# Kernel tuning notes

Hardware: AMD Instinct MI355X
Metric: run time of the kernel (lower is better)

The kernel has to match this reference:

```python
import jax, jax.numpy as jnp
import numpy as np

N_SEG = 16384      # number of ragged segments (customers)
SEG_LEN = 1024     # events per segment (uniform here; math supports ragged)
N = N_SEG * SEG_LEN
EPS = 1e-5


def setup_inputs() -> dict:
    key = jax.random.key(0)
    k1, k2 = jax.random.split(key)
    # tau = detached model prediction of next inter-event time; must be > 0
    tau = jax.random.uniform(k1, (N,), jnp.float32, 0.1, 2.0)
    # dt = observed inter-event times (non-negative)
    dt = jax.random.uniform(k2, (N,), jnp.float32, 0.0, 1.0)
    # offsets: B+1 boundaries of the ragged segments within the flat arrays
    offsets = jnp.arange(N_SEG + 1, dtype=jnp.int32) * SEG_LEN
    return {"tau": tau, "dt": dt, "offsets": offsets}


def reference(tau, dt, offsets):
    # Original loop: per segment, drop first and last event, accumulate
    # -log_prob under Exponential(rate=1/tau):
    #   -log_prob(x) = log(tau) + (dt + eps) / tau
    # Replaced by a single masked elementwise pass + sum: interior mask is
    # everything except each segment's first index and last index.
    n = dt.shape[0]
    mask = (
        jnp.ones((n,), dtype=bool)
        .at[offsets[:-1]].set(False)      # segment starts
        .at[offsets[1:] - 1].set(False)   # segment ends
    )
    tau_sg = jax.lax.stop_gradient(tau)   # y_pred['next_dt'].detach()
    nll = jnp.log(tau_sg) + (dt + EPS) / tau_sg
    loss = jnp.sum(jnp.where(mask, nll, jnp.zeros((), nll.dtype)))
    final_loss = loss / offsets.shape[0]  # divide by B+1, as in source
    return final_loss
```

## Files before the change

### kernel.cpp

```cpp
#include <hip/hip_runtime.h>

typedef float f32x4 __attribute__((ext_vector_type(4)));

#define EPS 1e-5f
#define THREADS 256
#define MAIN_BLOCKS 2048
#define SUPER 2048
#define BND_THREADS 256

#define GLOAD(dst, addr) \
  asm volatile("global_load_dwordx4 %0, %1, off" : "=v"(dst) : "v"(addr) : "memory")

#define SWAIT(n) \
  asm volatile("s_waitcnt vmcnt(" #n ")" ::: "memory"); \
  __builtin_amdgcn_sched_barrier(0)

#define NLL4(T, E) \
  a0 += __logf(T.x) + __fdividef(E.x + EPS, T.x); \
  a1 += __logf(T.y) + __fdividef(E.y + EPS, T.y); \
  a2 += __logf(T.z) + __fdividef(E.z + EPS, T.z); \
  a3 += __logf(T.w) + __fdividef(E.w + EPS, T.w)

#define ISSUE(T, E, P, Q) \
  GLOAD(T##0, P + 0 * THREADS); GLOAD(E##0, Q + 0 * THREADS); \
  GLOAD(T##1, P + 1 * THREADS); GLOAD(E##1, Q + 1 * THREADS); \
  GLOAD(T##2, P + 2 * THREADS); GLOAD(E##2, Q + 2 * THREADS); \
  GLOAD(T##3, P + 3 * THREADS); GLOAD(E##3, Q + 3 * THREADS); \
  GLOAD(T##4, P + 4 * THREADS); GLOAD(E##4, Q + 4 * THREADS); \
  GLOAD(T##5, P + 5 * THREADS); GLOAD(E##5, Q + 5 * THREADS); \
  GLOAD(T##6, P + 6 * THREADS); GLOAD(E##6, Q + 6 * THREADS); \
  GLOAD(T##7, P + 7 * THREADS); GLOAD(E##7, Q + 7 * THREADS)

#define COMPUTE16(T, E) \
  SWAIT(28); NLL4(T##0, E##0); NLL4(T##1, E##1); \
  SWAIT(24); NLL4(T##2, E##2); NLL4(T##3, E##3); \
  SWAIT(20); NLL4(T##4, E##4); NLL4(T##5, E##5); \
  SWAIT(16); NLL4(T##6, E##6); NLL4(T##7, E##7)

#define COMPUTE0(T, E) \
  SWAIT(12); NLL4(T##0, E##0); NLL4(T##1, E##1); \
  SWAIT(8);  NLL4(T##2, E##2); NLL4(T##3, E##3); \
  SWAIT(4);  NLL4(T##4, E##4); NLL4(T##5, E##5); \
  SWAIT(0);  NLL4(T##6, E##6); NLL4(T##7, E##7)

__global__ __launch_bounds__(THREADS, 2) void tau_loss_main(
    const f32x4* __restrict__ t4,
    const f32x4* __restrict__ d4,
    const float* __restrict__ tau,
    const float* __restrict__ dt,
    float* __restrict__ ws,
    int n) {
    const int n4 = n >> 2;
    const int nsuper = n4 / SUPER;

    float a0 = 0.f, a1 = 0.f, a2 = 0.f, a3 = 0.f;

    f32x4 tA0, tA1, tA2, tA3, tA4, tA5, tA6, tA7;
    f32x4 eA0, eA1, eA2, eA3, eA4, eA5, eA6, eA7;
    f32x4 tB0, tB1, tB2, tB3, tB4, tB5, tB6, tB7;
    f32x4 eB0, eB1, eB2, eB3, eB4, eB5, eB6, eB7;

    int s = (int)blockIdx.x;
    if (s < nsuper) {
        const f32x4* pt = t4 + s * SUPER + (int)threadIdx.x;
        const f32x4* pe = d4 + s * SUPER + (int)threadIdx.x;
        ISSUE(tA, eA, pt, pe);
        s += MAIN_BLOCKS;

        while (s < nsuper) {
            pt = t4 + s * SUPER + (int)threadIdx.x;
            pe = d4 + s * SUPER + (int)threadIdx.x;
            ISSUE(tB, eB, pt, pe);
            COMPUTE16(tA, eA);
            s += MAIN_BLOCKS;
            if (s < nsuper) {
                pt = t4 + s * SUPER + (int)threadIdx.x;
                pe = d4 + s * SUPER + (int)threadIdx.x;
                ISSUE(tA, eA, pt, pe);
                COMPUTE16(tB, eB);
                s += MAIN_BLOCKS;
            } else {
                COMPUTE0(tB, eB);
                goto main_done;
            }
        }
        COMPUTE0(tA, eA);
        main_done: ;
    }

    if (blockIdx.x == 0) {
        for (int i = nsuper * (SUPER * 4) + (int)threadIdx.x; i < n; i += THREADS) {
            float t = tau[i];
            a0 += __logf(t) + __fdividef(dt[i] + EPS, t);
        }
    }

    float acc = (a0 + a1) + (a2 + a3);

    #pragma unroll
    for (int off = 32; off > 0; off >>= 1)
        acc += __shfl_down(acc, off, 64);

    __shared__ float smem[THREADS / 64];
    int wave = threadIdx.x >> 6;
    int lane = threadIdx.x & 63;
    if (lane == 0) smem[wave] = acc;
    __syncthreads();
    if (threadIdx.x == 0)
        ws[blockIdx.x] = smem[0] + smem[1] + smem[2] + smem[3];
}

__global__ __launch_bounds__(BND_THREADS) void tau_loss_boundary(
    const float* __restrict__ tau,
    const float* __restrict__ dt,
    const int* __restrict__ offsets,
    float* __restrict__ ws,
    int nseg) {
    int k = blockIdx.x * blockDim.x + threadIdx.x;

    float sub = 0.0f;
    if (k < nseg) {
        int s = offsets[k];
        int e = offsets[k + 1] - 1;
        float ts = tau[s];
        sub = __logf(ts) + __fdividef(dt[s] + EPS, ts);
        if (e != s) {
            float te = tau[e];
            sub += __logf(te) + __fdividef(dt[e] + EPS, te);
        }
    }

    #pragma unroll
    for (int off = 32; off > 0; off >>= 1)
        sub += __shfl_down(sub, off, 64);

    __shared__ float smem[BND_THREADS / 64];
    int wave = threadIdx.x >> 6;
    int lane = threadIdx.x & 63;
    if (lane == 0) smem[wave] = sub;
    __syncthreads();
    if (threadIdx.x == 0)
        ws[MAIN_BLOCKS + blockIdx.x] = -(smem[0] + smem[1] + smem[2] + smem[3]);
}

__global__ __launch_bounds__(256) void tau_loss_final(
    const float* __restrict__ ws, int m, float inv_div,
    float* __restrict__ out) {
    float a = 0.f;
    for (int i = threadIdx.x; i < m; i += 256)
        a += ws[i];

    #pragma unroll
    for (int off = 32; off > 0; off >>= 1)
        a += __shfl_down(a, off, 64);

    __shared__ float smem[4];
    int wave = threadIdx.x >> 6;
    int lane = threadIdx.x & 63;
    if (lane == 0) smem[wave] = a;
    __syncthreads();
    if (threadIdx.x == 0)
        out[0] = (smem[0] + smem[1] + smem[2] + smem[3]) * inv_div;
}

extern "C" void kernel_launch(void* const* d_in, const int* in_sizes, int n_in,
                              void* d_out, int out_size, void* d_ws, size_t ws_size,
                              hipStream_t stream) {
    const float* tau = (const float*)d_in[0];
    const float* dt  = (const float*)d_in[1];
    const int* offsets = (const int*)d_in[2];
    float* out = (float*)d_out;
    float* ws = (float*)d_ws;

    const int n = in_sizes[0];
    const int n_off = in_sizes[2];
    const int nseg = n_off - 1;
    const float inv_div = 1.0f / (float)n_off;

    tau_loss_main<<<MAIN_BLOCKS, THREADS, 0, stream>>>(
        (const f32x4*)tau, (const f32x4*)dt, tau, dt, ws, n);

    int bblocks = (nseg + BND_THREADS - 1) / BND_THREADS;
    if (bblocks < 1) bblocks = 1;
    tau_loss_boundary<<<bblocks, BND_THREADS, 0, stream>>>(tau, dt, offsets, ws, nseg);

    tau_loss_final<<<1, 256, 0, stream>>>(ws, MAIN_BLOCKS + bblocks, inv_div, out);
}
```

Before: 32.82 us.

## Fuse boundary subtraction into main reduction kernel and halve main grid

```diff
diff --git a/kernel.cpp b/kernel.cpp
--- a/kernel.cpp
+++ b/kernel.cpp
@@ -4,9 +4,8 @@
 
 #define EPS 1e-5f
 #define THREADS 256
-#define MAIN_BLOCKS 2048
+#define MAIN_BLOCKS 1024
 #define SUPER 2048
-#define BND_THREADS 256
 
 #define GLOAD(dst, addr) \
   asm volatile("global_load_dwordx4 %0, %1, off" : "=v"(dst) : "v"(addr) : "memory")
@@ -43,13 +42,38 @@
   SWAIT(4);  NLL4(T##4, E##4); NLL4(T##5, E##5); \
   SWAIT(0);  NLL4(T##6, E##6); NLL4(T##7, E##7)
 
+__device__ __forceinline__ void subtract_boundaries(
+    const int* __restrict__ offsets, int nseg,
+    const float* __restrict__ tau, const float* __restrict__ dt,
+    int lo, int hi, float& acc) {
+    int L = 0, R = nseg;
+    while (L < R) { int m = (L + R) >> 1; if (offsets[m] < lo) L = m + 1; else R = m; }
+    for (int k = L + (int)threadIdx.x; k < nseg; k += THREADS) {
+        int s = offsets[k];
+        if (s >= hi) break;
+        float ts = tau[s];
+        acc -= __logf(ts) + __fdividef(dt[s] + EPS, ts);
+    }
+    L = 0; R = nseg;
+    while (L < R) { int m = (L + R) >> 1; if (offsets[m + 1] - 1 < lo) L = m + 1; else R = m; }
+    for (int k = L + (int)threadIdx.x; k < nseg; k += THREADS) {
+        int e = offsets[k + 1] - 1;
+        if (e >= hi) break;
+        if (e != offsets[k]) {
+            float te = tau[e];
+            acc -= __logf(te) + __fdividef(dt[e] + EPS, te);
+        }
+    }
+}
+
 __global__ __launch_bounds__(THREADS, 2) void tau_loss_main(
     const f32x4* __restrict__ t4,
     const f32x4* __restrict__ d4,
     const float* __restrict__ tau,
     const float* __restrict__ dt,
+    const int* __restrict__ offsets,
     float* __restrict__ ws,
-    int n) {
+    int n, int nseg) {
     const int n4 = n >> 2;
     const int nsuper = n4 / SUPER;
 
@@ -95,6 +119,13 @@
         }
     }
 
+    for (int q = (int)blockIdx.x; q < nsuper; q += MAIN_BLOCKS) {
+        int lo = q * (SUPER * 4);
+        subtract_boundaries(offsets, nseg, tau, dt, lo, lo + SUPER * 4, a0);
+    }
+    if (blockIdx.x == 0 && nsuper * (SUPER * 4) < n)
+        subtract_boundaries(offsets, nseg, tau, dt, nsuper * (SUPER * 4), n, a0);
+
     float acc = (a0 + a1) + (a2 + a3);
 
     #pragma unroll
@@ -108,39 +139,6 @@
     __syncthreads();
     if (threadIdx.x == 0)
         ws[blockIdx.x] = smem[0] + smem[1] + smem[2] + smem[3];
-}
-
-__global__ __launch_bounds__(BND_THREADS) void tau_loss_boundary(
-    const float* __restrict__ tau,
-    const float* __restrict__ dt,
-    const int* __restrict__ offsets,
-    float* __restrict__ ws,
-    int nseg) {
-    int k = blockIdx.x * blockDim.x + threadIdx.x;
-
-    float sub = 0.0f;
-    if (k < nseg) {
-        int s = offsets[k];
-        int e = offsets[k + 1] - 1;
-        float ts = tau[s];
-        sub = __logf(ts) + __fdividef(dt[s] + EPS, ts);
-        if (e != s) {
-            float te = tau[e];
-            sub += __logf(te) + __fdividef(dt[e] + EPS, te);
-        }
-    }
-
-    #pragma unroll
-    for (int off = 32; off > 0; off >>= 1)
-        sub += __shfl_down(sub, off, 64);
-
-    __shared__ float smem[BND_THREADS / 64];
-    int wave = threadIdx.x >> 6;
-    int lane = threadIdx.x & 63;
-    if (lane == 0) smem[wave] = sub;
-    __syncthreads();
-    if (threadIdx.x == 0)
-        ws[MAIN_BLOCKS + blockIdx.x] = -(smem[0] + smem[1] + smem[2] + smem[3]);
 }
 
 __global__ __launch_bounds__(256) void tau_loss_final(
@@ -178,11 +176,7 @@
     const float inv_div = 1.0f / (float)n_off;
 
     tau_loss_main<<<MAIN_BLOCKS, THREADS, 0, stream>>>(
-        (const f32x4*)tau, (const f32x4*)dt, tau, dt, ws, n);
+        (const f32x4*)tau, (const f32x4*)dt, tau, dt, offsets, ws, n, nseg);
 
-    int bblocks = (nseg + BND_THREADS - 1) / BND_THREADS;
-    if (bblocks < 1) bblocks = 1;
-    tau_loss_boundary<<<bblocks, BND_THREADS, 0, stream>>>(tau, dt, offsets, ws, nseg);
-
-    tau_loss_final<<<1, 256, 0, stream>>>(ws, MAIN_BLOCKS + bblocks, inv_div, out);
+    tau_loss_final<<<1, 256, 0, stream>>>(ws, MAIN_BLOCKS, inv_div, out);
 }
```

Measured after the change: 42.76 us. +30.3%, slower.
